# Optimization experiments

Measured on AMD Instinct MI355X. Metric: run time of the kernel, lower is better.

The kernel has to match this reference:

```python
import jax, jax.numpy as jnp
import numpy as np

H = 16  # num_heads (inner_dim 1024 // default head_dim 64)
D = 64  # head_dim
EPS = 1e-5

def layernorm(x, w, b):
    mu = jnp.mean(x, axis=-1, keepdims=True)
    var = jnp.var(x, axis=-1, keepdims=True)
    return (x - mu) * jax.lax.rsqrt(var + EPS) * w + b

def attention(x, kv, wq, wk, wv, wo, bo):
    b, t, c = x.shape
    s = kv.shape[1]
    q = (x @ wq).reshape(b, t, H, D).transpose(0, 2, 1, 3)   # bhtd
    k = (kv @ wk).reshape(b, s, H, D).transpose(0, 2, 1, 3)  # bhsd
    v = (kv @ wv).reshape(b, s, H, D).transpose(0, 2, 1, 3)
    scores = jnp.einsum('bhqd,bhkd->bhqk', q, k) * (D ** -0.5)
    attn = jax.nn.softmax(scores, axis=-1)
    out = jnp.einsum('bhqk,bhkd->bhqd', attn, v)
    out = out.transpose(0, 2, 1, 3).reshape(b, t, c)
    return out @ wo + bo

def setup_inputs() -> dict:
    key = jax.random.key(0)
    ks = jax.random.split(key, 16)
    hs = 1024
    dff = 4 * hs  # 4096
    sc = lambda fan_in: 1.0 / np.sqrt(fan_in)
    inp = {
        'x': jax.random.normal(ks[0], (2, 2048, hs), jnp.float32),
        'encoder_hidden_states': jax.random.normal(ks[1], (2, 512, 64), jnp.float32),
        'ln1_w': jnp.ones((hs,), jnp.float32), 'ln1_b': jnp.zeros((hs,), jnp.float32),
        'a1_wq': jax.random.normal(ks[2], (hs, hs), jnp.float32) * sc(hs),
        'a1_wk': jax.random.normal(ks[3], (hs, hs), jnp.float32) * sc(hs),
        'a1_wv': jax.random.normal(ks[4], (hs, hs), jnp.float32) * sc(hs),
        'a1_wo': jax.random.normal(ks[5], (hs, hs), jnp.float32) * sc(hs),
        'a1_bo': jnp.zeros((hs,), jnp.float32),
        'ln2_w': jnp.ones((hs,), jnp.float32), 'ln2_b': jnp.zeros((hs,), jnp.float32),
        'a2_wq': jax.random.normal(ks[6], (hs, hs), jnp.float32) * sc(hs),
        'a2_wk': jax.random.normal(ks[7], (64, hs), jnp.float32) * sc(64),
        'a2_wv': jax.random.normal(ks[8], (64, hs), jnp.float32) * sc(64),
        'a2_wo': jax.random.normal(ks[9], (hs, hs), jnp.float32) * sc(hs),
        'a2_bo': jnp.zeros((hs,), jnp.float32),
        'ln3_w': jnp.ones((hs,), jnp.float32), 'ln3_b': jnp.zeros((hs,), jnp.float32),
        'ff_w1': jax.random.normal(ks[10], (hs, 2 * dff), jnp.float32) * sc(hs),
        'ff_b1': jnp.zeros((2 * dff,), jnp.float32),
        'ff_w2': jax.random.normal(ks[11], (dff, hs), jnp.float32) * sc(dff),
        'ff_b2': jnp.zeros((hs,), jnp.float32),
    }
    return inp

def reference(x, encoder_hidden_states, ln1_w, ln1_b, a1_wq, a1_wk, a1_wv, a1_wo, a1_bo,
              ln2_w, ln2_b, a2_wq, a2_wk, a2_wv, a2_wo, a2_bo,
              ln3_w, ln3_b, ff_w1, ff_b1, ff_w2, ff_b2):
    # self-attention sub-block
    h = layernorm(x, ln1_w, ln1_b)
    x = x + attention(h, h, a1_wq, a1_wk, a1_wv, a1_wo, a1_bo)
    # cross-attention sub-block (kv from encoder_hidden_states, dim 64)
    h = layernorm(x, ln2_w, ln2_b)
    x = x + attention(h, encoder_hidden_states, a2_wq, a2_wk, a2_wv, a2_wo, a2_bo)
    # GEGLU feed-forward sub-block
    h = layernorm(x, ln3_w, ln3_b)
    hp = h @ ff_w1 + ff_b1
    h1, h2 = jnp.split(hp, 2, axis=-1)
    h = (h1 * jax.nn.gelu(h2, approximate=False)) @ ff_w2 + ff_b2
    return x + h
```

## Files before the change

### kernel.cpp

```cpp
#include <hip/hip_runtime.h>
#include <hip/hip_bf16.h>
#include <stdint.h>

typedef unsigned short u16;
typedef __bf16 bf16x8 __attribute__((ext_vector_type(8)));
typedef float f32x4 __attribute__((ext_vector_type(4)));
typedef u16 u16x8 __attribute__((ext_vector_type(8)));
typedef u16 u16x4 __attribute__((ext_vector_type(4)));

__device__ __forceinline__ u16 f2bf(float f) {
  union { float f; uint32_t u; } v; v.f = f;
  uint32_t r = v.u + 0x7fffu + ((v.u >> 16) & 1u);
  return (u16)(r >> 16);
}
__device__ __forceinline__ float bf2f(u16 u) {
  union { uint32_t u; float f; } v; v.u = ((uint32_t)u) << 16;
  return v.f;
}
__device__ __forceinline__ uint32_t cvtpk(float a, float b) {
  uint32_t r;
  asm("v_cvt_pk_bf16_f32 %0, %1, %2" : "=v"(r) : "v"(a), "v"(b));
  return r;
}

__device__ __forceinline__ void gld16(const u16* g, u16* l) {
  __builtin_amdgcn_global_load_lds(
      (const __attribute__((address_space(1))) uint32_t*)g,
      (__attribute__((address_space(3))) uint32_t*)l, 16, 0, 0);
}

__device__ __forceinline__ void stage_half(const u16* __restrict__ gbase, int ldg,
                                           u16* lbase, int tid) {
#pragma unroll
  for (int j = 0; j < 2; ++j) {
    const int idx = j * 512 + tid;
    const int row = idx >> 3, c8 = idx & 7;
    gld16(gbase + (size_t)row * ldg + ((c8 ^ (row & 7)) << 3), lbase + idx * 8);
  }
}

__global__ void wconv_t(const float* __restrict__ W, u16* __restrict__ Wt, int K, int N,
                        float scale) {
  __shared__ float tile[32][33];
  const int n0 = blockIdx.x * 32, k0 = blockIdx.y * 32;
  const int tx = threadIdx.x, ty = threadIdx.y;
#pragma unroll
  for (int i = 0; i < 4; ++i)
    tile[ty + 8 * i][tx] = W[(size_t)(k0 + ty + 8 * i) * N + n0 + tx];
  __syncthreads();
#pragma unroll
  for (int i = 0; i < 4; ++i)
    Wt[(size_t)(n0 + ty + 8 * i) * K + k0 + tx] = f2bf(scale * tile[tx][ty + 8 * i]);
}

__global__ void cvt_bf(const float* __restrict__ in, u16* __restrict__ out, int n) {
  int i = blockIdx.x * 256 + threadIdx.x;
  if (i < n) out[i] = f2bf(in[i]);
}

__global__ __launch_bounds__(256)
void vtrans(const u16* __restrict__ V, int ldv, int hoff, u16* __restrict__ Vt, int S) {
  __shared__ u16 tile[64][72];
  const int t0 = blockIdx.x, bh = blockIdx.y;
  const int b = bh >> 4, hc = (bh & 15) * 64 + hoff;
  const int tid = threadIdx.x;
  const int r = tid >> 2, dq = (tid & 3) * 16;
  const int pos = ((r >> 5) << 5) | (((r >> 2) & 3) << 3) | (((r >> 4) & 1) << 2) | (r & 3);
  const size_t grow = ((size_t)b * S + t0 * 64 + r) * ldv + hc + dq;
  u16x8 v1 = *(const u16x8*)&V[grow];
  u16x8 v2 = *(const u16x8*)&V[grow + 8];
#pragma unroll
  for (int j = 0; j < 8; ++j) {
    tile[dq + j][pos] = v1[j];
    tile[dq + 8 + j][pos] = v2[j];
  }
  __syncthreads();
  const int d = tid >> 2, c = (tid & 3) * 16;
  u16x8 o1, o2;
#pragma unroll
  for (int j = 0; j < 8; ++j) { o1[j] = tile[d][c + j]; o2[j] = tile[d][c + 8 + j]; }
  *(u16x8*)&Vt[((size_t)bh * 64 + d) * S + t0 * 64 + c] = o1;
  *(u16x8*)&Vt[((size_t)bh * 64 + d) * S + t0 * 64 + c + 8] = o2;
}

__global__ __launch_bounds__(256)
void ln_fwd(const float* __restrict__ X, const float* __restrict__ wt,
            const float* __restrict__ bs, u16* __restrict__ Y) {
  const int row = blockIdx.x, t = threadIdx.x;
  const float4 v = *(const float4*)&X[(size_t)row * 1024 + t * 4];
  float s = v.x + v.y + v.z + v.w;
  float s2 = v.x * v.x + v.y * v.y + v.z * v.z + v.w * v.w;
#pragma unroll
  for (int off = 32; off > 0; off >>= 1) {
    s += __shfl_xor(s, off);
    s2 += __shfl_xor(s2, off);
  }
  __shared__ float rs[4], rs2[4];
  const int w = t >> 6;
  if ((t & 63) == 0) { rs[w] = s; rs2[w] = s2; }
  __syncthreads();
  s = rs[0] + rs[1] + rs[2] + rs[3];
  s2 = rs2[0] + rs2[1] + rs2[2] + rs2[3];
  const float mu = s * (1.0f / 1024.0f);
  const float var = s2 * (1.0f / 1024.0f) - mu * mu;
  const float rstd = rsqrtf(var + 1e-5f);
  const float4 wv = *(const float4*)&wt[t * 4];
  const float4 bv = *(const float4*)&bs[t * 4];
  u16x4 o;
  o[0] = f2bf((v.x - mu) * rstd * wv.x + bv.x);
  o[1] = f2bf((v.y - mu) * rstd * wv.y + bv.y);
  o[2] = f2bf((v.z - mu) * rstd * wv.z + bv.z);
  o[3] = f2bf((v.w - mu) * rstd * wv.w + bv.w);
  *(u16x4*)&Y[(size_t)row * 1024 + t * 4] = o;
}

template<int TN>
__global__ __launch_bounds__(256, 2)
void gemm_bf16(const u16* __restrict__ A, int lda, const u16* __restrict__ Bt,
               int M, int N, int K, const float* __restrict__ bias,
               const float* __restrict__ resid, float oscale,
               float* __restrict__ outF, u16* __restrict__ outB) {
  constexpr int WNV = (TN == 128) ? 2 : 1;
  constexpr int WMV = 4 / WNV;
  constexpr int WM = 128 / WMV;
  constexpr int WN = TN / WNV;
  constexpr int MI = WM / 16, NI = WN / 16;
  __shared__ __align__(16) u16 Al[128 * 64];
  __shared__ __align__(16) u16 Bl[TN * 64];
  const int tid = threadIdx.x;
  const int w = tid >> 6, l = tid & 63, lo = l & 15, g = l >> 4;
  const int gx = gridDim.x, nwg = gx * gridDim.y;
  const int lin = blockIdx.y * gx + blockIdx.x;
  const int q = nwg >> 3, r = nwg & 7;
  const int xcd = lin & 7, pos = lin >> 3;
  const int sid = (xcd < r ? xcd * (q + 1) : r * (q + 1) + (xcd - r) * q) + pos;
  const int bm = (sid % gx) * 128, bn = (sid / gx) * TN;
  const int wm = (w / WNV) * WM, wn = (w % WNV) * WN;
  f32x4 acc[MI][NI] = {};

  for (int k0 = 0; k0 < K; k0 += 64) {
#pragma unroll
    for (int p = 0; p < 4; ++p) {
      int idx = p * 256 + tid;
      int row = idx >> 3, c = idx & 7;
      gld16(A + (size_t)(bm + row) * lda + k0 + c * 8, &Al[idx * 8]);
    }
#pragma unroll
    for (int p = 0; p < TN / 32; ++p) {
      int idx = p * 256 + tid;
      int row = idx >> 3, c = idx & 7;
      gld16(Bt + (size_t)(bn + row) * K + k0 + c * 8, &Bl[idx * 8]);
    }
    asm volatile("s_waitcnt vmcnt(0)" ::: "memory");
    __syncthreads();
#pragma unroll
    for (int ks = 0; ks < 2; ++ks) {
      bf16x8 af[MI], bf[NI];
#pragma unroll
      for (int i = 0; i < MI; ++i)
        af[i] = *(const bf16x8*)&Al[(wm + i * 16 + lo) * 64 + ks * 32 + g * 8];
#pragma unroll
      for (int i = 0; i < NI; ++i)
        bf[i] = *(const bf16x8*)&Bl[(wn + i * 16 + lo) * 64 + ks * 32 + g * 8];
#pragma unroll
      for (int mi = 0; mi < MI; ++mi)
#pragma unroll
        for (int ni = 0; ni < NI; ++ni)
          acc[mi][ni] = __builtin_amdgcn_mfma_f32_16x16x32_bf16(af[mi], bf[ni], acc[mi][ni], 0, 0, 0);
    }
    __syncthreads();
  }

#pragma unroll
  for (int mi = 0; mi < MI; ++mi) {
#pragma unroll
    for (int ni = 0; ni < NI; ++ni) {
      const int col = bn + wn + ni * 16 + lo;
      const float bb = bias ? bias[col] : 0.0f;
      const int row0 = bm + wm + mi * 16 + g * 4;
#pragma unroll
      for (int rr = 0; rr < 4; ++rr) {
        const size_t off = (size_t)(row0 + rr) * N + col;
        float v = acc[mi][ni][rr] * oscale + bb;
        if (resid) v += resid[off];
        if (outF) outF[off] = v;
        else outB[off] = f2bf(v);
      }
    }
  }
}

__global__ __launch_bounds__(512, 2)
void gemm256(const u16* __restrict__ A, int lda, const u16* __restrict__ Bt,
             int M, int N, int K, const float* __restrict__ bias,
             const float* __restrict__ resid, float oscale,
             float* __restrict__ outF, u16* __restrict__ outB) {
  __shared__ __align__(16) u16 sm[65536];
  const int tid = threadIdx.x;
  const int w = tid >> 6, l = tid & 63, lo = l & 15, g = l >> 4;
  const int wrow = w >> 2, wcol = w & 3;
  const int gx = gridDim.x;
  const int nwg = gx * gridDim.y;
  const int lin = blockIdx.y * gx + blockIdx.x;
  const int q = nwg >> 3, r = nwg & 7;
  const int xcd = lin & 7, pos = lin >> 3;
  const int sid = (xcd < r ? xcd * (q + 1) : r * (q + 1) + (xcd - r) * q) + pos;
  const int bm = (sid % gx) * 256, bn = (sid / gx) * 256;

  const int NT = K >> 6;
  const int swz = (lo & 7) << 3;
  f32x4 acc[8][4] = {};

  stage_half(Bt + (size_t)bn * K, K, sm + 16384, tid);
  stage_half(Bt + (size_t)(bn + 128) * K, K, sm + 16384 + 8192, tid);
  stage_half(A + (size_t)bm * lda, lda, sm, tid);
  stage_half(A + (size_t)(bm + 128) * lda, lda, sm + 8192, tid);
  if (NT > 1) {
    stage_half(Bt + (size_t)bn * K + 64, K, sm + 32768 + 16384, tid);
    stage_half(Bt + (size_t)(bn + 128) * K + 64, K, sm + 32768 + 16384 + 8192, tid);
    stage_half(A + (size_t)bm * lda + 64, lda, sm + 32768, tid);
  }
  asm volatile("s_waitcnt vmcnt(6)" ::: "memory");
  __builtin_amdgcn_s_barrier();

  for (int t = 0; t < NT; ++t) {
    u16* Ab_ = sm + (t & 1) * 32768;
    u16* Bb_ = Ab_ + 16384;
    bf16x8 a0[4][2], a1[4][2], bfr[4][2];
#pragma unroll
    for (int mf = 0; mf < 4; ++mf) {
      const int rowi = wrow * 128 + mf * 16 + lo;
#pragma unroll
      for (int kk = 0; kk < 2; ++kk)
        a0[mf][kk] = *(const bf16x8*)&Ab_[rowi * 64 + ((kk * 32 + g * 8) ^ swz)];
    }
#pragma unroll
    for (int nf = 0; nf < 4; ++nf) {
      const int rowi = wcol * 64 + nf * 16 + lo;
#pragma unroll
      for (int kk = 0; kk < 2; ++kk)
        bfr[nf][kk] = *(const bf16x8*)&Bb_[rowi * 64 + ((kk * 32 + g * 8) ^ swz)];
    }
    if (t + 1 < NT)
      stage_half(A + (size_t)(bm + 128) * lda + (t + 1) * 64, lda,
                 sm + ((t + 1) & 1) * 32768 + 8192, tid);
    __builtin_amdgcn_s_barrier();
    asm volatile("s_waitcnt lgkmcnt(0)" ::: "memory");
    __builtin_amdgcn_s_setprio(1);
#pragma unroll
    for (int mf = 0; mf < 4; ++mf)
#pragma unroll
      for (int nf = 0; nf < 2; ++nf)
#pragma unroll
        for (int kk = 0; kk < 2; ++kk)
          acc[mf][nf] = __builtin_amdgcn_mfma_f32_16x16x32_bf16(a0[mf][kk], bfr[nf][kk], acc[mf][nf], 0, 0, 0);
    __builtin_amdgcn_s_setprio(0);
    __builtin_amdgcn_s_barrier();
    if (t + 2 < NT)
      stage_half(Bt + (size_t)bn * K + (t + 2) * 64, K,
                 sm + (t & 1) * 32768 + 16384, tid);
    __builtin_amdgcn_s_barrier();
    __builtin_amdgcn_s_setprio(1);
#pragma unroll
    for (int mf = 0; mf < 4; ++mf)
#pragma unroll
      for (int nf = 2; nf < 4; ++nf)
#pragma unroll
        for (int kk = 0; kk < 2; ++kk)
          acc[mf][nf] = __builtin_amdgcn_mfma_f32_16x16x32_bf16(a0[mf][kk], bfr[nf][kk], acc[mf][nf], 0, 0, 0);
    __builtin_amdgcn_s_setprio(0);
    __builtin_amdgcn_s_barrier();
#pragma unroll
    for (int mf = 0; mf < 4; ++mf) {
      const int rowi = wrow * 128 + 64 + mf * 16 + lo;
#pragma unroll
      for (int kk = 0; kk < 2; ++kk)
        a1[mf][kk] = *(const bf16x8*)&Ab_[rowi * 64 + ((kk * 32 + g * 8) ^ swz)];
    }
    if (t + 2 < NT)
      stage_half(Bt + (size_t)(bn + 128) * K + (t + 2) * 64, K,
                 sm + (t & 1) * 32768 + 16384 + 8192, tid);
    __builtin_amdgcn_s_barrier();
    asm volatile("s_waitcnt lgkmcnt(0)" ::: "memory");
    __builtin_amdgcn_s_setprio(1);
#pragma unroll
    for (int mf = 0; mf < 4; ++mf)
#pragma unroll
      for (int nf = 0; nf < 2; ++nf)
#pragma unroll
        for (int kk = 0; kk < 2; ++kk)
          acc[4 + mf][nf] = __builtin_amdgcn_mfma_f32_16x16x32_bf16(a1[mf][kk], bfr[nf][kk], acc[4 + mf][nf], 0, 0, 0);
    __builtin_amdgcn_s_setprio(0);
    __builtin_amdgcn_s_barrier();
    if (t + 2 < NT)
      stage_half(A + (size_t)bm * lda + (t + 2) * 64, lda,
                 sm + (t & 1) * 32768, tid);
    __builtin_amdgcn_s_barrier();
    __builtin_amdgcn_s_setprio(1);
#pragma unroll
    for (int mf = 0; mf < 4; ++mf)
#pragma unroll
      for (int nf = 2; nf < 4; ++nf)
#pragma unroll
        for (int kk = 0; kk < 2; ++kk)
          acc[4 + mf][nf] = __builtin_amdgcn_mfma_f32_16x16x32_bf16(a1[mf][kk], bfr[nf][kk], acc[4 + mf][nf], 0, 0, 0);
    __builtin_amdgcn_s_setprio(0);
    if (t + 2 < NT) asm volatile("s_waitcnt vmcnt(6)" ::: "memory");
    else            asm volatile("s_waitcnt vmcnt(0)" ::: "memory");
    __builtin_amdgcn_s_barrier();
  }

#pragma unroll
  for (int mi = 0; mi < 8; ++mi) {
#pragma unroll
    for (int ni = 0; ni < 4; ++ni) {
      const int col = bn + wcol * 64 + ni * 16 + lo;
      const float bb = bias ? bias[col] : 0.0f;
      const int row0 = bm + wrow * 128 + mi * 16 + g * 4;
#pragma unroll
      for (int rr = 0; rr < 4; ++rr) {
        const size_t off = (size_t)(row0 + rr) * N + col;
        float v = acc[mi][ni][rr] * oscale + bb;
        if (resid) v += resid[off];
        if (outF) outF[off] = v;
        else outB[off] = f2bf(v);
      }
    }
  }
}

__global__ __launch_bounds__(256, 4)
void attn_fwd(const u16* __restrict__ Q, int ldq, const u16* __restrict__ K, int ldk,
              const u16* __restrict__ Vt, u16* __restrict__ O, int T, int S) {
  __shared__ __align__(16) u16 Kl[2][4096];
  __shared__ __align__(16) u16 Vl[2][4096];
  const int tid = threadIdx.x, w = tid >> 6, l = tid & 63, lo = l & 15, g = l >> 4;
  const int nwg = gridDim.x * gridDim.y;
  const int n = blockIdx.y * gridDim.x + blockIdx.x;
  const int sid = (n & 7) * (nwg >> 3) + (n >> 3);
  const int qt = sid % gridDim.x, bh = sid / gridDim.x;
  const int b = bh >> 4, h = bh & 15, hc = h * 64;
  const int q0 = qt * 64 + w * 16;
  const size_t qrow = (size_t)b * T + q0;
  const size_t krow0 = (size_t)b * S;
  const size_t vrow0 = (size_t)bh * 64;

  bf16x8 qf[2];
#pragma unroll
  for (int kk = 0; kk < 2; ++kk)
    qf[kk] = *(const bf16x8*)&Q[(qrow + lo) * ldq + hc + kk * 32 + g * 8];

  f32x4 oa[4] = {};
  float m = -1e30f, lsum = 0.0f;

  const int srow = tid >> 3;
  const int scol = (((tid & 7) ^ (srow & 7)) << 3);

  const int ntile = S >> 6;
#pragma unroll
  for (int c = 0; c < 2; ++c)
    gld16(K + (krow0 + c * 32 + srow) * ldk + hc + scol, &Kl[0][c * 2048 + tid * 8]);
#pragma unroll
  for (int c = 0; c < 2; ++c)
    gld16(Vt + (vrow0 + c * 32 + srow) * S + scol, &Vl[0][c * 2048 + tid * 8]);

  for (int t0 = 0; t0 < ntile; ++t0) {
    const int cur = t0 & 1;
    if (t0 + 1 < ntile) {
      const int nxt = cur ^ 1;
#pragma unroll
      for (int c = 0; c < 2; ++c)
        gld16(K + (krow0 + (t0 + 1) * 64 + c * 32 + srow) * ldk + hc + scol,
              &Kl[nxt][c * 2048 + tid * 8]);
#pragma unroll
      for (int c = 0; c < 2; ++c)
        gld16(Vt + (vrow0 + c * 32 + srow) * S + (t0 + 1) * 64 + scol,
              &Vl[nxt][c * 2048 + tid * 8]);
      asm volatile("s_waitcnt vmcnt(4)" ::: "memory");
    } else {
      asm volatile("s_waitcnt vmcnt(0)" ::: "memory");
    }
    __builtin_amdgcn_s_barrier();

    f32x4 s[4] = {};
#pragma unroll
    for (int c = 0; c < 4; ++c)
#pragma unroll
      for (int kk = 0; kk < 2; ++kk) {
        bf16x8 kf = *(const bf16x8*)&Kl[cur][(c * 16 + lo) * 64 +
                                            ((kk * 32 + g * 8) ^ ((lo & 7) << 3))];
        s[c] = __builtin_amdgcn_mfma_f32_16x16x32_bf16(kf, qf[kk], s[c], 0, 0, 0);
      }

    float mx = fmaxf(fmaxf(fmaxf(s[0][0], s[0][1]), fmaxf(s[0][2], s[0][3])),
                     fmaxf(fmaxf(s[1][0], s[1][1]), fmaxf(s[1][2], s[1][3])));
    mx = fmaxf(mx, fmaxf(fmaxf(fmaxf(s[2][0], s[2][1]), fmaxf(s[2][2], s[2][3])),
                         fmaxf(fmaxf(s[3][0], s[3][1]), fmaxf(s[3][2], s[3][3]))));
    mx = fmaxf(mx, __shfl_xor(mx, 16));
    mx = fmaxf(mx, __shfl_xor(mx, 32));
    const float mn = fmaxf(m, mx);
    const float al = exp2f(m - mn);
    m = mn;
    float psum = 0.0f;
#pragma unroll
    for (int c = 0; c < 4; ++c)
#pragma unroll
      for (int rr = 0; rr < 4; ++rr) {
        s[c][rr] = exp2f(s[c][rr] - mn);
        psum += s[c][rr];
      }
    psum += __shfl_xor(psum, 16);
    psum += __shfl_xor(psum, 32);
    lsum = lsum * al + psum;
    f32x4 arv;
#pragma unroll
    for (int rr = 0; rr < 4; ++rr) arv[rr] = __shfl(al, 20 * g + rr);
#pragma unroll
    for (int dn = 0; dn < 4; ++dn) oa[dn] *= arv;

    union { uint32_t u[4]; bf16x8 v; } af[2];
#pragma unroll
    for (int ks = 0; ks < 2; ++ks) {
      af[ks].u[0] = cvtpk(s[2 * ks][0], s[2 * ks][1]);
      af[ks].u[1] = cvtpk(s[2 * ks][2], s[2 * ks][3]);
      af[ks].u[2] = cvtpk(s[2 * ks + 1][0], s[2 * ks + 1][1]);
      af[ks].u[3] = cvtpk(s[2 * ks + 1][2], s[2 * ks + 1][3]);
    }
#pragma unroll
    for (int dn = 0; dn < 4; ++dn)
#pragma unroll
      for (int ks = 0; ks < 2; ++ks) {
        bf16x8 vf = *(const bf16x8*)&Vl[cur][(dn * 16 + lo) * 64 +
                                            ((ks * 32 + g * 8) ^ ((lo & 7) << 3))];
        oa[dn] = __builtin_amdgcn_mfma_f32_16x16x32_bf16(af[ks].v, vf, oa[dn], 0, 0, 0);
      }
    asm volatile("s_waitcnt lgkmcnt(0)" ::: "memory");
    __builtin_amdgcn_s_barrier();
  }

  const float il = 1.0f / lsum;
  float ir[4];
#pragma unroll
  for (int rr = 0; rr < 4; ++rr) ir[rr] = __shfl(il, 20 * g + rr);
#pragma unroll
  for (int dn = 0; dn < 4; ++dn)
#pragma unroll
    for (int rr = 0; rr < 4; ++rr)
      O[(qrow + g * 4 + rr) * 1024 + hc + dn * 16 + lo] = f2bf(oa[dn][rr] * ir[rr]);
}

__global__ __launch_bounds__(256)
void geglu_k(u16* __restrict__ hp) {
  const size_t i = (size_t)blockIdx.x * 256 + threadIdx.x;
  const int row = (int)(i >> 9), c8 = (int)(i & 511);
  u16* p1 = hp + (size_t)row * 8192 + c8 * 8;
  const u16* p2 = p1 + 4096;
  u16x8 a = *(const u16x8*)p1;
  u16x8 bq = *(const u16x8*)p2;
  u16x8 o;
#pragma unroll
  for (int j = 0; j < 8; ++j) {
    float x1 = bf2f(a[j]), x2 = bf2f(bq[j]);
    float ge = 0.5f * x2 * (1.0f + erff(x2 * 0.70710678118f));
    o[j] = f2bf(x1 * ge);
  }
  *(u16x8*)p1 = o;
}

extern "C" void kernel_launch(void* const* d_in, const int* in_sizes, int n_in,
                              void* d_out, int out_size, void* d_ws, size_t ws_size,
                              hipStream_t stream) {
  const float* x      = (const float*)d_in[0];
  const float* enc    = (const float*)d_in[1];
  const float* ln1_w  = (const float*)d_in[2];
  const float* ln1_b  = (const float*)d_in[3];
  const float* a1_wq  = (const float*)d_in[4];
  const float* a1_wk  = (const float*)d_in[5];
  const float* a1_wv  = (const float*)d_in[6];
  const float* a1_wo  = (const float*)d_in[7];
  const float* a1_bo  = (const float*)d_in[8];
  const float* ln2_w  = (const float*)d_in[9];
  const float* ln2_b  = (const float*)d_in[10];
  const float* a2_wq  = (const float*)d_in[11];
  const float* a2_wk  = (const float*)d_in[12];
  const float* a2_wv  = (const float*)d_in[13];
  const float* a2_wo  = (const float*)d_in[14];
  const float* a2_bo  = (const float*)d_in[15];
  const float* ln3_w  = (const float*)d_in[16];
  const float* ln3_b  = (const float*)d_in[17];
  const float* ff_w1  = (const float*)d_in[18];
  const float* ff_b1  = (const float*)d_in[19];
  const float* ff_w2  = (const float*)d_in[20];
  const float* ff_b2  = (const float*)d_in[21];

  char* ws = (char*)d_ws;
  const size_t MB = 1u << 20;
  u16* wqkv1t = (u16*)(ws + 0 * MB);
  u16* wo1t   = (u16*)(ws + 6 * MB);
  u16* wq2t   = (u16*)(ws + 8 * MB);
  u16* wo2t   = (u16*)(ws + 10 * MB);
  u16* wk2t   = (u16*)(ws + 12 * MB);
  u16* wv2t   = (u16*)(ws + 12 * MB + 256 * 1024);
  u16* encb   = (u16*)(ws + 12 * MB + 512 * 1024);
  u16* w1t    = (u16*)(ws + 13 * MB);
  u16* w2t    = (u16*)(ws + 29 * MB);
  float* x2   = (float*)(ws + 37 * MB);
  u16* Vt1    = (u16*)(ws + 37 * MB);
  u16* Vt2    = (u16*)(ws + 45 * MB);
  u16* hbuf   = (u16*)(ws + 53 * MB);
  u16* qkv    = (u16*)(ws + 61 * MB);
  u16* Qb     = (u16*)(ws + 61 * MB);
  u16* Kb     = (u16*)(ws + 69 * MB);
  u16* Vb     = (u16*)(ws + 77 * MB);
  u16* Ab     = (u16*)(ws + 85 * MB);
  float* x1   = (float*)(ws + 93 * MB);
  u16* hp     = (u16*)(ws + 61 * MB);

  const float SCL = 0.125f * 1.44269504f;
  const dim3 tb(32, 8);
  wconv_t<<<dim3(32, 32), tb, 0, stream>>>(a1_wq, wqkv1t, 1024, 1024, SCL);
  wconv_t<<<dim3(32, 32), tb, 0, stream>>>(a1_wk, wqkv1t + 1024 * 1024, 1024, 1024, 1.0f);
  wconv_t<<<dim3(32, 32), tb, 0, stream>>>(a1_wv, wqkv1t + 2048 * 1024, 1024, 1024, 1.0f);
  wconv_t<<<dim3(32, 32), tb, 0, stream>>>(a1_wo, wo1t, 1024, 1024, 1.0f);
  wconv_t<<<dim3(32, 32), tb, 0, stream>>>(a2_wq, wq2t, 1024, 1024, SCL);
  wconv_t<<<dim3(32, 2),  tb, 0, stream>>>(a2_wk, wk2t, 64, 1024, 1.0f);
  wconv_t<<<dim3(32, 2),  tb, 0, stream>>>(a2_wv, wv2t, 64, 1024, 1.0f);
  wconv_t<<<dim3(32, 32), tb, 0, stream>>>(a2_wo, wo2t, 1024, 1024, 1.0f);
  wconv_t<<<dim3(256, 32), tb, 0, stream>>>(ff_w1, w1t, 1024, 8192, 1.0f);
  wconv_t<<<dim3(32, 128), tb, 0, stream>>>(ff_w2, w2t, 4096, 1024, 1.0f);
  cvt_bf<<<256, 256, 0, stream>>>(enc, encb, 2 * 512 * 64);

  ln_fwd<<<4096, 256, 0, stream>>>(x, ln1_w, ln1_b, hbuf);
  gemm256<<<dim3(16, 12), 512, 0, stream>>>(hbuf, 1024, wqkv1t, 4096, 3072, 1024, nullptr, nullptr, 1.0f, nullptr, qkv);
  vtrans<<<dim3(32, 32), 256, 0, stream>>>(qkv, 3072, 2048, Vt1, 2048);
  attn_fwd<<<dim3(32, 32), 256, 0, stream>>>(qkv, 3072, qkv + 1024, 3072, Vt1, Ab, 2048, 2048);
  gemm_bf16<64><<<dim3(32, 16), 256, 0, stream>>>(Ab, 1024, wo1t, 4096, 1024, 1024, a1_bo, x, 1.0f, x1, nullptr);

  ln_fwd<<<4096, 256, 0, stream>>>(x1, ln2_w, ln2_b, hbuf);
  gemm_bf16<64><<<dim3(32, 16), 256, 0, stream>>>(hbuf, 1024, wq2t, 4096, 1024, 1024, nullptr, nullptr, 1.0f, nullptr, Qb);
  gemm_bf16<64><<<dim3(8, 16), 256, 0, stream>>>(encb, 64, wk2t, 1024, 1024, 64, nullptr, nullptr, 1.0f, nullptr, Kb);
  gemm_bf16<64><<<dim3(8, 16), 256, 0, stream>>>(encb, 64, wv2t, 1024, 1024, 64, nullptr, nullptr, 1.0f, nullptr, Vb);
  vtrans<<<dim3(8, 32), 256, 0, stream>>>(Vb, 1024, 0, Vt2, 512);
  attn_fwd<<<dim3(32, 32), 256, 0, stream>>>(Qb, 1024, Kb, 1024, Vt2, Ab, 2048, 512);
  gemm_bf16<64><<<dim3(32, 16), 256, 0, stream>>>(Ab, 1024, wo2t, 4096, 1024, 1024, a2_bo, x1, 1.0f, x2, nullptr);

  ln_fwd<<<4096, 256, 0, stream>>>(x2, ln3_w, ln3_b, hbuf);
  gemm256<<<dim3(16, 32), 512, 0, stream>>>(hbuf, 1024, w1t, 4096, 8192, 1024, ff_b1, nullptr, 1.0f, nullptr, hp);
  geglu_k<<<8192, 256, 0, stream>>>(hp);
  gemm_bf16<64><<<dim3(32, 16), 256, 0, stream>>>(hp, 8192, w2t, 4096, 1024, 4096, ff_b2, x2, 1.0f, (float*)d_out, nullptr);
}
```

Measured before the change: 479.3 us.

## Fuse GEGLU into FF1 GEMM epilogue, batch weight conversions, merge cross-attn K/V GEMMs

The FF1 weight is written interleaved so each 256-column GEMM tile holds matching h1 and h2 halves. The GEMM epilogue then computes gelu(h2)*h1 through LDS and writes only the 4096-wide product, which removes the separate geglu kernel and the full hp round trip. Weight conversions are batched into one launch via blockIdx.z, and the cross-attention K and V projections are merged into one GEMM. The gemm256 main loop also splits the B fragments into two sets with partial lgkmcnt waits to overlap LDS reads with MFMAs. The costs are more epilogue register and LDS pressure and several unrelated changes bundled together.

```diff
diff --git a/kernel.cpp b/kernel.cpp
--- a/kernel.cpp
+++ b/kernel.cpp
@@ -39,8 +39,16 @@
   }
 }
 
-__global__ void wconv_t(const float* __restrict__ W, u16* __restrict__ Wt, int K, int N,
-                        float scale) {
+struct WB {
+  const float* src[6];
+  u16* dst[6];
+  float scale[6];
+};
+__global__ void wconv_b(WB wb, int K, int N) {
+  const int z = blockIdx.z;
+  const float* __restrict__ W = wb.src[z];
+  u16* __restrict__ Wt = wb.dst[z];
+  const float scale = wb.scale[z];
   __shared__ float tile[32][33];
   const int n0 = blockIdx.x * 32, k0 = blockIdx.y * 32;
   const int tx = threadIdx.x, ty = threadIdx.y;
@@ -51,6 +59,35 @@
 #pragma unroll
   for (int i = 0; i < 4; ++i)
     Wt[(size_t)(n0 + ty + 8 * i) * K + k0 + tx] = f2bf(scale * tile[tx][ty + 8 * i]);
+}
+
+__global__ void wconv_t(const float* __restrict__ W, u16* __restrict__ Wt, int K, int N) {
+  __shared__ float tile[32][33];
+  const int n0 = blockIdx.x * 32, k0 = blockIdx.y * 32;
+  const int tx = threadIdx.x, ty = threadIdx.y;
+#pragma unroll
+  for (int i = 0; i < 4; ++i)
+    tile[ty + 8 * i][tx] = W[(size_t)(k0 + ty + 8 * i) * N + n0 + tx];
+  __syncthreads();
+#pragma unroll
+  for (int i = 0; i < 4; ++i)
+    Wt[(size_t)(n0 + ty + 8 * i) * K + k0 + tx] = f2bf(tile[tx][ty + 8 * i]);
+}
+
+__global__ void wconv_g(const float* __restrict__ W, u16* __restrict__ Wt) {
+  __shared__ float tile[32][33];
+  const int n0 = blockIdx.x * 32, k0 = blockIdx.y * 32;
+  const int tx = threadIdx.x, ty = threadIdx.y;
+#pragma unroll
+  for (int i = 0; i < 4; ++i)
+    tile[ty + 8 * i][tx] = W[(size_t)(k0 + ty + 8 * i) * 8192 + n0 + tx];
+  __syncthreads();
+#pragma unroll
+  for (int i = 0; i < 4; ++i) {
+    const int n = n0 + ty + 8 * i;
+    const int p = (((n & 4095) >> 7) << 8) + (((n >> 12) & 1) << 7) + (n & 127);
+    Wt[(size_t)p * 1024 + k0 + tx] = f2bf(tile[tx][ty + 8 * i]);
+  }
 }
 
 __global__ void cvt_bf(const float* __restrict__ in, u16* __restrict__ out, int n) {
@@ -190,6 +227,7 @@
   }
 }
 
+template<int MODE>
 __global__ __launch_bounds__(512, 2)
 void gemm256(const u16* __restrict__ A, int lda, const u16* __restrict__ Bt,
              int M, int N, int K, const float* __restrict__ bias,
@@ -226,7 +264,7 @@
   for (int t = 0; t < NT; ++t) {
     u16* Ab_ = sm + (t & 1) * 32768;
     u16* Bb_ = Ab_ + 16384;
-    bf16x8 a0[4][2], a1[4][2], bfr[4][2];
+    bf16x8 a0[4][2], a1[4][2], b01[2][2], b23[2][2];
 #pragma unroll
     for (int mf = 0; mf < 4; ++mf) {
       const int rowi = wrow * 128 + mf * 16 + lo;
@@ -235,17 +273,27 @@
         a0[mf][kk] = *(const bf16x8*)&Ab_[rowi * 64 + ((kk * 32 + g * 8) ^ swz)];
     }
 #pragma unroll
-    for (int nf = 0; nf < 4; ++nf) {
+    for (int nf = 0; nf < 2; ++nf) {
       const int rowi = wcol * 64 + nf * 16 + lo;
 #pragma unroll
       for (int kk = 0; kk < 2; ++kk)
-        bfr[nf][kk] = *(const bf16x8*)&Bb_[rowi * 64 + ((kk * 32 + g * 8) ^ swz)];
-    }
+        b01[nf][kk] = *(const bf16x8*)&Bb_[rowi * 64 + ((kk * 32 + g * 8) ^ swz)];
+    }
+    __builtin_amdgcn_sched_barrier(0);
+#pragma unroll
+    for (int nf = 0; nf < 2; ++nf) {
+      const int rowi = wcol * 64 + 32 + nf * 16 + lo;
+#pragma unroll
+      for (int kk = 0; kk < 2; ++kk)
+        b23[nf][kk] = *(const bf16x8*)&Bb_[rowi * 64 + ((kk * 32 + g * 8) ^ swz)];
+    }
+    __builtin_amdgcn_sched_barrier(0);
     if (t + 1 < NT)
       stage_half(A + (size_t)(bm + 128) * lda + (t + 1) * 64, lda,
                  sm + ((t + 1) & 1) * 32768 + 8192, tid);
     __builtin_amdgcn_s_barrier();
-    asm volatile("s_waitcnt lgkmcnt(0)" ::: "memory");
+    asm volatile("s_waitcnt lgkmcnt(4)" ::: "memory");
+    __builtin_amdgcn_sched_barrier(0);
     __builtin_amdgcn_s_setprio(1);
 #pragma unroll
     for (int mf = 0; mf < 4; ++mf)
@@ -253,35 +301,39 @@
       for (int nf = 0; nf < 2; ++nf)
 #pragma unroll
         for (int kk = 0; kk < 2; ++kk)
-          acc[mf][nf] = __builtin_amdgcn_mfma_f32_16x16x32_bf16(a0[mf][kk], bfr[nf][kk], acc[mf][nf], 0, 0, 0);
+          acc[mf][nf] = __builtin_amdgcn_mfma_f32_16x16x32_bf16(a0[mf][kk], b01[nf][kk], acc[mf][nf], 0, 0, 0);
     __builtin_amdgcn_s_setprio(0);
     __builtin_amdgcn_s_barrier();
+#pragma unroll
+    for (int mf = 0; mf < 4; ++mf) {
+      const int rowi = wrow * 128 + 64 + mf * 16 + lo;
+#pragma unroll
+      for (int kk = 0; kk < 2; ++kk)
+        a1[mf][kk] = *(const bf16x8*)&Ab_[rowi * 64 + ((kk * 32 + g * 8) ^ swz)];
+    }
+    __builtin_amdgcn_sched_barrier(0);
     if (t + 2 < NT)
       stage_half(Bt + (size_t)bn * K + (t + 2) * 64, K,
                  sm + (t & 1) * 32768 + 16384, tid);
     __builtin_amdgcn_s_barrier();
+    asm volatile("s_waitcnt lgkmcnt(8)" ::: "memory");
+    __builtin_amdgcn_sched_barrier(0);
     __builtin_amdgcn_s_setprio(1);
 #pragma unroll
     for (int mf = 0; mf < 4; ++mf)
 #pragma unroll
-      for (int nf = 2; nf < 4; ++nf)
+      for (int nf = 0; nf < 2; ++nf)
 #pragma unroll
         for (int kk = 0; kk < 2; ++kk)
-          acc[mf][nf] = __builtin_amdgcn_mfma_f32_16x16x32_bf16(a0[mf][kk], bfr[nf][kk], acc[mf][nf], 0, 0, 0);
+          acc[mf][2 + nf] = __builtin_amdgcn_mfma_f32_16x16x32_bf16(a0[mf][kk], b23[nf][kk], acc[mf][2 + nf], 0, 0, 0);
     __builtin_amdgcn_s_setprio(0);
     __builtin_amdgcn_s_barrier();
-#pragma unroll
-    for (int mf = 0; mf < 4; ++mf) {
-      const int rowi = wrow * 128 + 64 + mf * 16 + lo;
-#pragma unroll
-      for (int kk = 0; kk < 2; ++kk)
-        a1[mf][kk] = *(const bf16x8*)&Ab_[rowi * 64 + ((kk * 32 + g * 8) ^ swz)];
-    }
     if (t + 2 < NT)
       stage_half(Bt + (size_t)(bn + 128) * K + (t + 2) * 64, K,
                  sm + (t & 1) * 32768 + 16384 + 8192, tid);
     __builtin_amdgcn_s_barrier();
     asm volatile("s_waitcnt lgkmcnt(0)" ::: "memory");
+    __builtin_amdgcn_sched_barrier(0);
     __builtin_amdgcn_s_setprio(1);
 #pragma unroll
     for (int mf = 0; mf < 4; ++mf)
@@ -289,7 +341,7 @@
       for (int nf = 0; nf < 2; ++nf)
 #pragma unroll
         for (int kk = 0; kk < 2; ++kk)
-          acc[4 + mf][nf] = __builtin_amdgcn_mfma_f32_16x16x32_bf16(a1[mf][kk], bfr[nf][kk], acc[4 + mf][nf], 0, 0, 0);
+          acc[4 + mf][nf] = __builtin_amdgcn_mfma_f32_16x16x32_bf16(a1[mf][kk], b01[nf][kk], acc[4 + mf][nf], 0, 0, 0);
     __builtin_amdgcn_s_setprio(0);
     __builtin_amdgcn_s_barrier();
     if (t + 2 < NT)
@@ -300,14 +352,51 @@
 #pragma unroll
     for (int mf = 0; mf < 4; ++mf)
 #pragma unroll
-      for (int nf = 2; nf < 4; ++nf)
+      for (int nf = 0; nf < 2; ++nf)
 #pragma unroll
         for (int kk = 0; kk < 2; ++kk)
-          acc[4 + mf][nf] = __builtin_amdgcn_mfma_f32_16x16x32_bf16(a1[mf][kk], bfr[nf][kk], acc[4 + mf][nf], 0, 0, 0);
+          acc[4 + mf][2 + nf] = __builtin_amdgcn_mfma_f32_16x16x32_bf16(a1[mf][kk], b23[nf][kk], acc[4 + mf][2 + nf], 0, 0, 0);
     __builtin_amdgcn_s_setprio(0);
     if (t + 2 < NT) asm volatile("s_waitcnt vmcnt(6)" ::: "memory");
     else            asm volatile("s_waitcnt vmcnt(0)" ::: "memory");
     __builtin_amdgcn_s_barrier();
+  }
+
+  if (MODE == 1) {
+    float* smf = (float*)sm;
+    const int obase = bn >> 1;
+    if (wcol >= 2) {
+#pragma unroll
+      for (int mi = 0; mi < 8; ++mi)
+#pragma unroll
+        for (int ni = 0; ni < 4; ++ni) {
+          const int lc = (wcol - 2) * 64 + ni * 16 + lo;
+          const float bb = bias[4096 + obase + lc];
+#pragma unroll
+          for (int rr = 0; rr < 4; ++rr) {
+            const int rowi = wrow * 128 + mi * 16 + g * 4 + rr;
+            const float h2 = acc[mi][ni][rr] + bb;
+            smf[rowi * 128 + lc] = 0.5f * h2 * (1.0f + erff(h2 * 0.70710678118f));
+          }
+        }
+    }
+    __syncthreads();
+    if (wcol < 2) {
+#pragma unroll
+      for (int mi = 0; mi < 8; ++mi)
+#pragma unroll
+        for (int ni = 0; ni < 4; ++ni) {
+          const int lc = wcol * 64 + ni * 16 + lo;
+          const float bb = bias[obase + lc];
+#pragma unroll
+          for (int rr = 0; rr < 4; ++rr) {
+            const int rowi = wrow * 128 + mi * 16 + g * 4 + rr;
+            const float h1 = acc[mi][ni][rr] + bb;
+            outB[(size_t)(bm + rowi) * 4096 + obase + lc] = f2bf(h1 * smf[rowi * 128 + lc]);
+          }
+        }
+    }
+    return;
   }
 
 #pragma unroll
@@ -447,24 +536,6 @@
 #pragma unroll
     for (int rr = 0; rr < 4; ++rr)
       O[(qrow + g * 4 + rr) * 1024 + hc + dn * 16 + lo] = f2bf(oa[dn][rr] * ir[rr]);
-}
-
-__global__ __launch_bounds__(256)
-void geglu_k(u16* __restrict__ hp) {
-  const size_t i = (size_t)blockIdx.x * 256 + threadIdx.x;
-  const int row = (int)(i >> 9), c8 = (int)(i & 511);
-  u16* p1 = hp + (size_t)row * 8192 + c8 * 8;
-  const u16* p2 = p1 + 4096;
-  u16x8 a = *(const u16x8*)p1;
-  u16x8 bq = *(const u16x8*)p2;
-  u16x8 o;
-#pragma unroll
-  for (int j = 0; j < 8; ++j) {
-    float x1 = bf2f(a[j]), x2 = bf2f(bq[j]);
-    float ge = 0.5f * x2 * (1.0f + erff(x2 * 0.70710678118f));
-    o[j] = f2bf(x1 * ge);
-  }
-  *(u16x8*)p1 = o;
 }
 
 extern "C" void kernel_launch(void* const* d_in, const int* in_sizes, int n_in,
@@ -499,53 +570,59 @@
   u16* wo1t   = (u16*)(ws + 6 * MB);
   u16* wq2t   = (u16*)(ws + 8 * MB);
   u16* wo2t   = (u16*)(ws + 10 * MB);
-  u16* wk2t   = (u16*)(ws + 12 * MB);
-  u16* wv2t   = (u16*)(ws + 12 * MB + 256 * 1024);
+  u16* wkv2t  = (u16*)(ws + 12 * MB);
   u16* encb   = (u16*)(ws + 12 * MB + 512 * 1024);
   u16* w1t    = (u16*)(ws + 13 * MB);
   u16* w2t    = (u16*)(ws + 29 * MB);
   float* x2   = (float*)(ws + 37 * MB);
   u16* Vt1    = (u16*)(ws + 37 * MB);
   u16* Vt2    = (u16*)(ws + 45 * MB);
+  u16* KVb    = (u16*)(ws + 47 * MB);
   u16* hbuf   = (u16*)(ws + 53 * MB);
   u16* qkv    = (u16*)(ws + 61 * MB);
   u16* Qb     = (u16*)(ws + 61 * MB);
-  u16* Kb     = (u16*)(ws + 69 * MB);
-  u16* Vb     = (u16*)(ws + 77 * MB);
   u16* Ab     = (u16*)(ws + 85 * MB);
   float* x1   = (float*)(ws + 93 * MB);
-  u16* hp     = (u16*)(ws + 61 * MB);
+  u16* gq     = (u16*)(ws + 61 * MB);
 
   const float SCL = 0.125f * 1.44269504f;
   const dim3 tb(32, 8);
-  wconv_t<<<dim3(32, 32), tb, 0, stream>>>(a1_wq, wqkv1t, 1024, 1024, SCL);
-  wconv_t<<<dim3(32, 32), tb, 0, stream>>>(a1_wk, wqkv1t + 1024 * 1024, 1024, 1024, 1.0f);
-  wconv_t<<<dim3(32, 32), tb, 0, stream>>>(a1_wv, wqkv1t + 2048 * 1024, 1024, 1024, 1.0f);
-  wconv_t<<<dim3(32, 32), tb, 0, stream>>>(a1_wo, wo1t, 1024, 1024, 1.0f);
-  wconv_t<<<dim3(32, 32), tb, 0, stream>>>(a2_wq, wq2t, 1024, 1024, SCL);
-  wconv_t<<<dim3(32, 2),  tb, 0, stream>>>(a2_wk, wk2t, 64, 1024, 1.0f);
-  wconv_t<<<dim3(32, 2),  tb, 0, stream>>>(a2_wv, wv2t, 64, 1024, 1.0f);
-  wconv_t<<<dim3(32, 32), tb, 0, stream>>>(a2_wo, wo2t, 1024, 1024, 1.0f);
-  wconv_t<<<dim3(256, 32), tb, 0, stream>>>(ff_w1, w1t, 1024, 8192, 1.0f);
-  wconv_t<<<dim3(32, 128), tb, 0, stream>>>(ff_w2, w2t, 4096, 1024, 1.0f);
+  {
+    WB wb;
+    wb.src[0] = a1_wq; wb.dst[0] = wqkv1t;               wb.scale[0] = SCL;
+    wb.src[1] = a1_wk; wb.dst[1] = wqkv1t + 1024 * 1024; wb.scale[1] = 1.0f;
+    wb.src[2] = a1_wv; wb.dst[2] = wqkv1t + 2048 * 1024; wb.scale[2] = 1.0f;
+    wb.src[3] = a1_wo; wb.dst[3] = wo1t;                 wb.scale[3] = 1.0f;
+    wb.src[4] = a2_wq; wb.dst[4] = wq2t;                 wb.scale[4] = SCL;
+    wb.src[5] = a2_wo; wb.dst[5] = wo2t;                 wb.scale[5] = 1.0f;
+    wconv_b<<<dim3(32, 32, 6), tb, 0, stream>>>(wb, 1024, 1024);
+    WB wb2;
+    wb2.src[0] = a2_wk; wb2.dst[0] = wkv2t;             wb2.scale[0] = 1.0f;
+    wb2.src[1] = a2_wv; wb2.dst[1] = wkv2t + 64 * 1024; wb2.scale[1] = 1.0f;
+    wb2.src[2] = a2_wk; wb2.dst[2] = wkv2t;             wb2.scale[2] = 1.0f;
+    wb2.src[3] = a2_wk; wb2.dst[3] = wkv2t;             wb2.scale[3] = 1.0f;
+    wb2.src[4] = a2_wk; wb2.dst[4] = wkv2t;             wb2.scale[4] = 1.0f;
+    wb2.src[5] = a2_wk; wb2.dst[5] = wkv2t;             wb2.scale[5] = 1.0f;
+    wconv_b<<<dim3(32, 2, 2), tb, 0, stream>>>(wb2, 64, 1024);
+  }
+  wconv_g<<<dim3(256, 32), tb, 0, stream>>>(ff_w1, w1t);
+  wconv_t<<<dim3(32, 128), tb, 0, stream>>>(ff_w2, w2t, 4096, 1024);
   cvt_bf<<<256, 256, 0, stream>>>(enc, encb, 2 * 512 * 64);
 
   ln_fwd<<<4096, 256, 0, stream>>>(x, ln1_w, ln1_b, hbuf);
-  gemm256<<<dim3(16, 12), 512, 0, stream>>>(hbuf, 1024, wqkv1t, 4096, 3072, 1024, nullptr, nullptr, 1.0f, nullptr, qkv);
+  gemm256<0><<<dim3(16, 12), 512, 0, stream>>>(hbuf, 1024, wqkv1t, 4096, 3072, 1024, nullptr, nullptr, 1.0f, nullptr, qkv);
   vtrans<<<dim3(32, 32), 256, 0, stream>>>(qkv, 3072, 2048, Vt1, 2048);
   attn_fwd<<<dim3(32, 32), 256, 0, stream>>>(qkv, 3072, qkv + 1024, 3072, Vt1, Ab, 2048, 2048);
   gemm_bf16<64><<<dim3(32, 16), 256, 0, stream>>>(Ab, 1024, wo1t, 4096, 1024, 1024, a1_bo, x, 1.0f, x1, nullptr);
 
   ln_fwd<<<4096, 256, 0, stream>>>(x1, ln2_w, ln2_b, hbuf);
   gemm_bf16<64><<<dim3(32, 16), 256, 0, stream>>>(hbuf, 1024, wq2t, 4096, 1024, 1024, nullptr, nullptr, 1.0f, nullptr, Qb);
-  gemm_bf16<64><<<dim3(8, 16), 256, 0, stream>>>(encb, 64, wk2t, 1024, 1024, 64, nullptr, nullptr, 1.0f, nullptr, Kb);
-  gemm_bf16<64><<<dim3(8, 16), 256, 0, stream>>>(encb, 64, wv2t, 1024, 1024, 64, nullptr, nullptr, 1.0f, nullptr, Vb);
-  vtrans<<<dim3(8, 32), 256, 0, stream>>>(Vb, 1024, 0, Vt2, 512);
-  attn_fwd<<<dim3(32, 32), 256, 0, stream>>>(Qb, 1024, Kb, 1024, Vt2, Ab, 2048, 512);
+  gemm_bf16<64><<<dim3(8, 32), 256, 0, stream>>>(encb, 64, wkv2t, 1024, 2048, 64, nullptr, nullptr, 1.0f, nullptr, KVb);
+  vtrans<<<dim3(8, 32), 256, 0, stream>>>(KVb + 1024, 2048, 0, Vt2, 512);
+  attn_fwd<<<dim3(32, 32), 256, 0, stream>>>(Qb, 1024, KVb, 2048, Vt2, Ab, 2048, 512);
   gemm_bf16<64><<<dim3(32, 16), 256, 0, stream>>>(Ab, 1024, wo2t, 4096, 1024, 1024, a2_bo, x1, 1.0f, x2, nullptr);
 
   ln_fwd<<<4096, 256, 0, stream>>>(x2, ln3_w, ln3_b, hbuf);
-  gemm256<<<dim3(16, 32), 512, 0, stream>>>(hbuf, 1024, w1t, 4096, 8192, 1024, ff_b1, nullptr, 1.0f, nullptr, hp);
-  geglu_k<<<8192, 256, 0, stream>>>(hp);
-  gemm_bf16<64><<<dim3(32, 16), 256, 0, stream>>>(hp, 8192, w2t, 4096, 1024, 4096, ff_b2, x2, 1.0f, (float*)d_out, nullptr);
-}
+  gemm256<1><<<dim3(16, 32), 512, 0, stream>>>(hbuf, 1024, w1t, 4096, 8192, 1024, ff_b1, nullptr, 1.0f, nullptr, gq);
+  gemm_bf16<64><<<dim3(32, 16), 256, 0, stream>>>(gq, 4096, w2t, 4096, 1024, 4096, ff_b2, x2, 1.0f, (float*)d_out, nullptr);
+}
```

Result: faster. 468.7 us (-2.2%).
